# Kernel tuning notes

Hardware: AMD Instinct MI355X
Metric: run time of the kernel (lower is better)

## Reference

```python
import jax, jax.numpy as jnp
import numpy as np
from jax import lax

B, C, H, W = 8, 128, 256, 256
Q = 3            # polynomial order of SuperONN2d
K = 3            # kernel size
OC = C // 2      # SuperONN2d out channels
EPS = 1e-5       # LayerNorm eps (torch default)


def setup_inputs() -> dict:
    key = jax.random.key(0)
    k1, k2, k3 = jax.random.split(key, 3)
    x = jax.random.normal(k1, (B, C, H, W), dtype=jnp.float32)
    gamma = jnp.ones((C,), dtype=jnp.float32)
    beta = jnp.zeros((C,), dtype=jnp.float32)
    # SuperONN2d weight: (out_ch, q*in_ch, k, k), bias=False
    fan_in = Q * C * K * K
    Wc = jax.random.uniform(k2, (OC, Q * C, K, K), dtype=jnp.float32,
                            minval=-1.0, maxval=1.0) / np.sqrt(fan_in)
    return {"x": x, "gamma": gamma, "beta": beta, "Wc": Wc}


def _pixel_unshuffle2(y):
    # torch.nn.PixelUnshuffle(2): (B,C,H,W) -> (B,4C,H/2,W/2)
    b, c, h, w = y.shape
    y = y.reshape(b, c, h // 2, 2, w // 2, 2)
    y = y.transpose(0, 1, 3, 5, 2, 4)
    return y.reshape(b, c * 4, h // 2, w // 2)


def reference(x, gamma, beta, Wc):
    # LayerNormNLP2d: normalize over channel dim at each pixel
    mu = jnp.mean(x, axis=1, keepdims=True)
    var = jnp.mean(jnp.square(x - mu), axis=1, keepdims=True)
    xn = (x - mu) * lax.rsqrt(var + EPS)
    xn = xn * gamma[None, :, None, None] + beta[None, :, None, None]
    # SuperONN2d: concat powers x^1..x^Q on channels, then a single conv (no bias)
    xp = jnp.concatenate([xn ** (i + 1) for i in range(Q)], axis=1)  # (B, Q*C, H, W)
    y = lax.conv_general_dilated(
        xp, Wc, window_strides=(1, 1), padding=[(K // 2, K // 2)] * 2,
        dimension_numbers=("NCHW", "OIHW", "NCHW"))                  # (B, OC, H, W)
    return _pixel_unshuffle2(y)                                       # (B, 2C, H/2, W/2)
```

## Files before the change

kernel.cpp:

```cpp
#include <hip/hip_runtime.h>
#include <hip/hip_bf16.h>
#include <stdint.h>

#define BB   8
#define CCH  128
#define HH   256
#define WWD  256
#define OCC  64
#define HWW  (HH*WWD)
#define PLANE (BB*HWW*32)

typedef __attribute__((ext_vector_type(8)))  short  bf16x8;
typedef __attribute__((ext_vector_type(16))) float  f32x16;
typedef __attribute__((ext_vector_type(4)))  unsigned int u32x4;
typedef __attribute__((ext_vector_type(2)))  float  f32x2;

static __device__ __forceinline__ unsigned cvt_pk_bf16(float lo, float hi) {
    unsigned r;
    asm("v_cvt_pk_bf16_f32 %0, %1, %2" : "=v"(r) : "v"(lo), "v"(hi));
    return r;
}
static __device__ __forceinline__ float bf16lo_to_f(unsigned u) {
    union { unsigned u; float f; } c; c.u = u << 16; return c.f;
}
static __device__ __forceinline__ float bf16hi_to_f(unsigned u) {
    union { unsigned u; float f; } c; c.u = u & 0xffff0000u; return c.f;
}

__global__ void prep_w(const float* __restrict__ Wc, unsigned short* __restrict__ Wb3) {
    int t = blockIdx.x * 256 + threadIdx.x;
    int lane = t & 63;
    int f    = t >> 6;
    int nt   = f & 1;
    int kh   = (f >> 1) & 1;
    int cc   = (f >> 2) & 3;
    int tq   = f >> 4;
    int q    = tq % 3;
    int tap  = tq / 3;
    int oc   = nt * 32 + (lane & 31);
    int kb   = cc * 32 + kh * 16 + (lane >> 5) * 8;
    u32x4 o;
    #pragma unroll
    for (int k = 0; k < 4; ++k) {
        float v0 = Wc[(size_t)(oc * 384 + q * 128 + kb + 2 * k) * 9 + tap];
        float v1 = Wc[(size_t)(oc * 384 + q * 128 + kb + 2 * k + 1) * 9 + tap];
        o[k] = cvt_pk_bf16(v0, v1);
    }
    *(u32x4*)(Wb3 + (size_t)t * 8) = o;
}

__global__ __launch_bounds__(256) void ln_kernel(
        const float* __restrict__ x, const float* __restrict__ gamma,
        const float* __restrict__ beta, unsigned short* __restrict__ xn2) {
    int p  = blockIdx.x * 256 + threadIdx.x;
    int b  = p >> 16;
    int hw = p & 65535;
    const float* xb = x + (size_t)b * CCH * HWW + hw;
    unsigned buf[64];
    float sum = 0.f, sumsq = 0.f;
    #pragma unroll
    for (int cp = 0; cp < 64; ++cp) {
        float v0 = xb[(size_t)(2 * cp) * HWW];
        float v1 = xb[(size_t)(2 * cp + 1) * HWW];
        sum   += v0 + v1;
        sumsq += v0 * v0 + v1 * v1;
        buf[cp] = cvt_pk_bf16(v0, v1);
    }
    float mu  = sum * (1.f / 128.f);
    float var = sumsq * (1.f / 128.f) - mu * mu;
    float rs  = rsqrtf(var + 1e-5f);
    size_t pix = (size_t)p * 32;
    #pragma unroll
    for (int g = 0; g < 16; ++g) {
        u32x4 o;
        #pragma unroll
        for (int k = 0; k < 4; ++k) {
            int cp = g * 4 + k;
            float f0 = bf16lo_to_f(buf[cp]);
            float f1 = bf16hi_to_f(buf[cp]);
            int c0 = cp * 2, c1 = cp * 2 + 1;
            float y0 = fmaf((f0 - mu) * rs, gamma[c0], beta[c0]);
            float y1 = fmaf((f1 - mu) * rs, gamma[c1], beta[c1]);
            o[k] = cvt_pk_bf16(y0, y1);
        }
        *(u32x4*)(xn2 + (size_t)(g >> 2) * PLANE + pix + (g & 3) * 8) = o;
    }
}

__global__ __launch_bounds__(256, 2) void conv_kernel(
        const unsigned short* __restrict__ xn2,
        const unsigned short* __restrict__ Wb3,
        float* __restrict__ out) {
    __shared__ __align__(16) unsigned char P[10 * 12 * 34 * 16];

    int bid = blockIdx.x;
    int bx  = bid & 7;
    int by  = (bid >> 3) & 31;
    int b   = bid >> 8;
    int x0  = bx * 32;
    int y0  = by * 8;
    int tid  = threadIdx.x;
    int lane = tid & 63;
    int w    = tid >> 6;
    int l31  = lane & 31;
    int kb   = lane >> 5;

    f32x16 acc[2][2];
    #pragma unroll
    for (int mt = 0; mt < 2; ++mt)
        #pragma unroll
        for (int nt = 0; nt < 2; ++nt)
            #pragma unroll
            for (int r = 0; r < 16; ++r)
                acc[mt][nt][r] = 0.f;

    int offg[6];
    int woff[6];
    bool vldf[6], wrf[6];
    #pragma unroll
    for (int it = 0; it < 6; ++it) {
        int item = tid + it * 256;
        bool ok  = item < 1360;
        int ii   = ok ? item : 0;
        int row  = ii / 136;
        int rem  = ii - row * 136;
        int px   = rem >> 2;
        int g2   = rem & 3;
        int yy   = y0 - 1 + row;
        int xx   = x0 - 1 + px;
        bool inb = ok && (unsigned)yy < 256u && (unsigned)xx < 256u;
        offg[it] = (yy * 256 + xx) * 32 + g2 * 8;
        woff[it] = (row * 12 + g2) * 34 + px;
        vldf[it] = inb;
        wrf[it]  = ok;
    }

    const unsigned short* xpb = xn2 + (size_t)b * HWW * 32;
    const bf16x8* wlane = (const bf16x8*)Wb3 + lane;
    const unsigned char* pa = P + ((size_t)kb * 34 + l31) * 16;

    u32x4 rs[6];
    #pragma unroll
    for (int it = 0; it < 6; ++it) {
        u32x4 v = (u32x4){0u, 0u, 0u, 0u};
        if (vldf[it]) v = *(const u32x4*)(xpb + offg[it]);
        rs[it] = v;
    }

    #pragma unroll 1
    for (int cc = 0; cc < 4; ++cc) {
        if (cc > 0) __syncthreads();
        #pragma unroll
        for (int it = 0; it < 6; ++it) {
            if (!wrf[it]) continue;
            u32x4 u1 = rs[it];
            u32x4 u2, u3;
            #pragma unroll
            for (int k = 0; k < 4; ++k) {
                float f0 = bf16lo_to_f(u1[k]);
                float f1 = bf16hi_to_f(u1[k]);
                float s0 = f0 * f0, s1 = f1 * f1;
                u2[k] = cvt_pk_bf16(s0, s1);
                u3[k] = cvt_pk_bf16(s0 * f0, s1 * f1);
            }
            unsigned char* cell = P + (size_t)woff[it] * 16;
            *(u32x4*)(cell)            = u1;
            *(u32x4*)(cell + 4*34*16)  = u2;
            *(u32x4*)(cell + 8*34*16)  = u3;
        }
        __syncthreads();

        if (cc < 3) {
            const unsigned short* xpn = xpb + (size_t)(cc + 1) * PLANE;
            #pragma unroll
            for (int it = 0; it < 6; ++it) {
                u32x4 v = (u32x4){0u, 0u, 0u, 0u};
                if (vldf[it]) v = *(const u32x4*)(xpn + offg[it]);
                rs[it] = v;
            }
        }

        const bf16x8* wcc = wlane + (size_t)cc * 4 * 64;
        bf16x8 av[2][2][2], bv[2][2][2];
        #pragma unroll
        for (int mt = 0; mt < 2; ++mt)
            #pragma unroll
            for (int kh = 0; kh < 2; ++kh)
                av[0][mt][kh] = *(const bf16x8*)(pa
                    + (size_t)(((2 * w + mt) * 12 + kh * 2) * 34) * 16);
        #pragma unroll
        for (int nt = 0; nt < 2; ++nt)
            #pragma unroll
            for (int kh = 0; kh < 2; ++kh)
                bv[0][nt][kh] = wcc[(kh * 2 + nt) * 64];

        #pragma unroll
        for (int tq = 0; tq < 27; ++tq) {
            const int cur = tq & 1, nxt = cur ^ 1;
            if (tq < 26) {
                const int t2 = tq + 1;
                const int ky = t2 / 9, kx = (t2 / 3) % 3, q = t2 % 3;
                #pragma unroll
                for (int mt = 0; mt < 2; ++mt)
                    #pragma unroll
                    for (int kh = 0; kh < 2; ++kh)
                        av[nxt][mt][kh] = *(const bf16x8*)(pa
                            + (size_t)((((2 * w + mt + ky) * 12 + q * 4 + kh * 2) * 34)
                                       + kx) * 16);
                #pragma unroll
                for (int nt = 0; nt < 2; ++nt)
                    #pragma unroll
                    for (int kh = 0; kh < 2; ++kh)
                        bv[nxt][nt][kh] = wcc[((size_t)t2 * 16 + kh * 2 + nt) * 64];
            }
            __builtin_amdgcn_s_setprio(1);
            #pragma unroll
            for (int kh = 0; kh < 2; ++kh)
                #pragma unroll
                for (int nt = 0; nt < 2; ++nt)
                    #pragma unroll
                    for (int mt = 0; mt < 2; ++mt)
                        acc[mt][nt] = __builtin_amdgcn_mfma_f32_32x32x16_bf16(
                            av[cur][mt][kh], bv[cur][nt][kh], acc[mt][nt], 0, 0, 0);
            __builtin_amdgcn_s_setprio(0);
        }
    }

    #pragma unroll
    for (int mt = 0; mt < 2; ++mt) {
        int y  = y0 + 2 * w + mt;
        int s  = mt;
        int y2 = y >> 1;
        #pragma unroll
        for (int nt = 0; nt < 2; ++nt) {
            int oc = nt * 32 + l31;
            #pragma unroll
            for (int p = 0; p < 8; ++p) {
                const int r  = (p & 1) + (p >> 1) * 4;
                int px = (r & 3) + 8 * (r >> 2) + 4 * kb;
                int x  = x0 + px;
                int ch = oc * 4 + s * 2 + (x & 1);
                int x2 = x >> 1;
                size_t off = ((size_t)(b * 256 + ch) * 128 + y2) * 128 + x2;
                f32x2 v;
                v.x = acc[mt][nt][r];
                v.y = acc[mt][nt][r + 2];
                *(f32x2*)(out + off) = v;
            }
        }
    }
}

extern "C" void kernel_launch(void* const* d_in, const int* in_sizes, int n_in,
                              void* d_out, int out_size, void* d_ws, size_t ws_size,
                              hipStream_t stream) {
    const float* x     = (const float*)d_in[0];
    const float* gamma = (const float*)d_in[1];
    const float* beta  = (const float*)d_in[2];
    const float* Wc    = (const float*)d_in[3];
    float* out = (float*)d_out;

    const size_t xn_bytes = (size_t)4 * PLANE * 2;
    const size_t wb_bytes = (size_t)27648 * 16;
    if (ws_size < xn_bytes + wb_bytes) return;
    unsigned short* xn2 = (unsigned short*)d_ws;
    unsigned short* Wb3 = (unsigned short*)((char*)d_ws + xn_bytes);

    hipLaunchKernelGGL(prep_w, dim3(108), dim3(256), 0, stream, Wc, Wb3);
    hipLaunchKernelGGL(ln_kernel, dim3(2048), dim3(256), 0, stream, x, gamma, beta, xn2);
    hipLaunchKernelGGL(conv_kernel, dim3(2048), dim3(256), 0, stream, xn2, Wb3, out);
}
```

Before: 326.1 us.

## Use taller conv tiles with 16-channel sub-chunks for more weight reuse

The conv tile grows from 8 to 16 output rows per block, and each wave now handles 4 M-tiles instead of 2, so every weight B-fragment feeds 4 MFMAs. Channel chunks shrink from 32 to 16 so the LDS halo tile stays about the same size. The weight prepack layout is reordered to match, and the grid is halved. The aim is less halo reloading and less weight traffic per output. The cost is more accumulator registers, twice as many barriers and fill phases, and fewer blocks, which may hurt occupancy or latency hiding.

```diff
diff --git a/kernel.cpp b/kernel.cpp
--- a/kernel.cpp
+++ b/kernel.cpp
@@ -9,6 +9,8 @@
 #define OCC  64
 #define HWW  (HH*WWD)
 #define PLANE (BB*HWW*32)
+#define NLD  1224
+#define QSTR (2*34)
 
 typedef __attribute__((ext_vector_type(8)))  short  bf16x8;
 typedef __attribute__((ext_vector_type(16))) float  f32x16;
@@ -27,26 +29,25 @@
     union { unsigned u; float f; } c; c.u = u & 0xffff0000u; return c.f;
 }
 
-__global__ void prep_w(const float* __restrict__ Wc, unsigned short* __restrict__ Wb3) {
+__global__ void prep_w(const float* __restrict__ Wc, unsigned short* __restrict__ Wb4) {
     int t = blockIdx.x * 256 + threadIdx.x;
     int lane = t & 63;
     int f    = t >> 6;
     int nt   = f & 1;
-    int kh   = (f >> 1) & 1;
-    int cc   = (f >> 2) & 3;
+    int sc   = (f >> 1) & 7;
     int tq   = f >> 4;
     int q    = tq % 3;
     int tap  = tq / 3;
     int oc   = nt * 32 + (lane & 31);
-    int kb   = cc * 32 + kh * 16 + (lane >> 5) * 8;
+    int cb   = sc * 16 + (lane >> 5) * 8;
     u32x4 o;
     #pragma unroll
     for (int k = 0; k < 4; ++k) {
-        float v0 = Wc[(size_t)(oc * 384 + q * 128 + kb + 2 * k) * 9 + tap];
-        float v1 = Wc[(size_t)(oc * 384 + q * 128 + kb + 2 * k + 1) * 9 + tap];
+        float v0 = Wc[(size_t)(oc * 384 + q * 128 + cb + 2 * k) * 9 + tap];
+        float v1 = Wc[(size_t)(oc * 384 + q * 128 + cb + 2 * k + 1) * 9 + tap];
         o[k] = cvt_pk_bf16(v0, v1);
     }
-    *(u32x4*)(Wb3 + (size_t)t * 8) = o;
+    *(u32x4*)(Wb4 + (size_t)t * 8) = o;
 }
 
 __global__ __launch_bounds__(256) void ln_kernel(
@@ -89,71 +90,71 @@
 
 __global__ __launch_bounds__(256, 2) void conv_kernel(
         const unsigned short* __restrict__ xn2,
-        const unsigned short* __restrict__ Wb3,
+        const unsigned short* __restrict__ Wb4,
         float* __restrict__ out) {
-    __shared__ __align__(16) unsigned char P[10 * 12 * 34 * 16];
+    __shared__ __align__(16) unsigned char P[18 * 6 * 34 * 16];
 
     int bid = blockIdx.x;
     int bx  = bid & 7;
-    int by  = (bid >> 3) & 31;
-    int b   = bid >> 8;
+    int by  = (bid >> 3) & 15;
+    int b   = bid >> 7;
     int x0  = bx * 32;
-    int y0  = by * 8;
+    int y0  = by * 16;
     int tid  = threadIdx.x;
     int lane = tid & 63;
     int w    = tid >> 6;
     int l31  = lane & 31;
     int kb   = lane >> 5;
 
-    f32x16 acc[2][2];
-    #pragma unroll
-    for (int mt = 0; mt < 2; ++mt)
+    f32x16 acc[4][2];
+    #pragma unroll
+    for (int mt = 0; mt < 4; ++mt)
         #pragma unroll
         for (int nt = 0; nt < 2; ++nt)
             #pragma unroll
             for (int r = 0; r < 16; ++r)
                 acc[mt][nt][r] = 0.f;
 
-    int offg[6];
-    int woff[6];
-    bool vldf[6], wrf[6];
-    #pragma unroll
-    for (int it = 0; it < 6; ++it) {
+    int offg[5];
+    int woff[5];
+    bool vldf[5], wrf[5];
+    #pragma unroll
+    for (int it = 0; it < 5; ++it) {
         int item = tid + it * 256;
-        bool ok  = item < 1360;
+        bool ok  = item < NLD;
         int ii   = ok ? item : 0;
-        int row  = ii / 136;
-        int rem  = ii - row * 136;
-        int px   = rem >> 2;
-        int g2   = rem & 3;
+        int row  = ii / 68;
+        int rem  = ii - row * 68;
+        int g    = rem / 34;
+        int px   = rem - g * 34;
         int yy   = y0 - 1 + row;
         int xx   = x0 - 1 + px;
         bool inb = ok && (unsigned)yy < 256u && (unsigned)xx < 256u;
-        offg[it] = (yy * 256 + xx) * 32 + g2 * 8;
-        woff[it] = (row * 12 + g2) * 34 + px;
+        offg[it] = (yy * 256 + xx) * 32 + g * 8;
+        woff[it] = (row * 6 + g) * 34 + px;
         vldf[it] = inb;
         wrf[it]  = ok;
     }
 
     const unsigned short* xpb = xn2 + (size_t)b * HWW * 32;
-    const bf16x8* wlane = (const bf16x8*)Wb3 + lane;
+    const bf16x8* wlane = (const bf16x8*)Wb4 + lane;
     const unsigned char* pa = P + ((size_t)kb * 34 + l31) * 16;
 
-    u32x4 rs[6];
-    #pragma unroll
-    for (int it = 0; it < 6; ++it) {
+    u32x4 rsv[5];
+    #pragma unroll
+    for (int it = 0; it < 5; ++it) {
         u32x4 v = (u32x4){0u, 0u, 0u, 0u};
         if (vldf[it]) v = *(const u32x4*)(xpb + offg[it]);
-        rs[it] = v;
+        rsv[it] = v;
     }
 
     #pragma unroll 1
-    for (int cc = 0; cc < 4; ++cc) {
-        if (cc > 0) __syncthreads();
-        #pragma unroll
-        for (int it = 0; it < 6; ++it) {
+    for (int sc = 0; sc < 8; ++sc) {
+        if (sc > 0) __syncthreads();
+        #pragma unroll
+        for (int it = 0; it < 5; ++it) {
             if (!wrf[it]) continue;
-            u32x4 u1 = rs[it];
+            u32x4 u1 = rsv[it];
             u32x4 u2, u3;
             #pragma unroll
             for (int k = 0; k < 4; ++k) {
@@ -164,35 +165,32 @@
                 u3[k] = cvt_pk_bf16(s0 * f0, s1 * f1);
             }
             unsigned char* cell = P + (size_t)woff[it] * 16;
-            *(u32x4*)(cell)            = u1;
-            *(u32x4*)(cell + 4*34*16)  = u2;
-            *(u32x4*)(cell + 8*34*16)  = u3;
+            *(u32x4*)(cell)                  = u1;
+            *(u32x4*)(cell + QSTR * 16)      = u2;
+            *(u32x4*)(cell + 2 * QSTR * 16)  = u3;
         }
         __syncthreads();
 
-        if (cc < 3) {
-            const unsigned short* xpn = xpb + (size_t)(cc + 1) * PLANE;
-            #pragma unroll
-            for (int it = 0; it < 6; ++it) {
+        if (sc < 7) {
+            const int scn = sc + 1;
+            const unsigned short* xpn = xpb + (size_t)(scn >> 1) * PLANE
+                                            + (scn & 1) * 16;
+            #pragma unroll
+            for (int it = 0; it < 5; ++it) {
                 u32x4 v = (u32x4){0u, 0u, 0u, 0u};
                 if (vldf[it]) v = *(const u32x4*)(xpn + offg[it]);
-                rs[it] = v;
-            }
-        }
-
-        const bf16x8* wcc = wlane + (size_t)cc * 4 * 64;
-        bf16x8 av[2][2][2], bv[2][2][2];
-        #pragma unroll
-        for (int mt = 0; mt < 2; ++mt)
-            #pragma unroll
-            for (int kh = 0; kh < 2; ++kh)
-                av[0][mt][kh] = *(const bf16x8*)(pa
-                    + (size_t)(((2 * w + mt) * 12 + kh * 2) * 34) * 16);
+                rsv[it] = v;
+            }
+        }
+
+        const bf16x8* wsc = wlane + (size_t)sc * 2 * 64;
+        bf16x8 av[2][4], bv[2][2];
+        #pragma unroll
+        for (int mt = 0; mt < 4; ++mt)
+            av[0][mt] = *(const bf16x8*)(pa + (size_t)((4 * w + mt) * 6 * 34) * 16);
         #pragma unroll
         for (int nt = 0; nt < 2; ++nt)
-            #pragma unroll
-            for (int kh = 0; kh < 2; ++kh)
-                bv[0][nt][kh] = wcc[(kh * 2 + nt) * 64];
+            bv[0][nt] = wsc[nt * 64];
 
         #pragma unroll
         for (int tq = 0; tq < 27; ++tq) {
@@ -201,35 +199,28 @@
                 const int t2 = tq + 1;
                 const int ky = t2 / 9, kx = (t2 / 3) % 3, q = t2 % 3;
                 #pragma unroll
-                for (int mt = 0; mt < 2; ++mt)
-                    #pragma unroll
-                    for (int kh = 0; kh < 2; ++kh)
-                        av[nxt][mt][kh] = *(const bf16x8*)(pa
-                            + (size_t)((((2 * w + mt + ky) * 12 + q * 4 + kh * 2) * 34)
-                                       + kx) * 16);
+                for (int mt = 0; mt < 4; ++mt)
+                    av[nxt][mt] = *(const bf16x8*)(pa
+                        + (size_t)(((4 * w + mt + ky) * 6 + q * 2) * 34 + kx) * 16);
                 #pragma unroll
                 for (int nt = 0; nt < 2; ++nt)
-                    #pragma unroll
-                    for (int kh = 0; kh < 2; ++kh)
-                        bv[nxt][nt][kh] = wcc[((size_t)t2 * 16 + kh * 2 + nt) * 64];
+                    bv[nxt][nt] = wsc[((size_t)t2 * 16 + nt) * 64];
             }
             __builtin_amdgcn_s_setprio(1);
             #pragma unroll
-            for (int kh = 0; kh < 2; ++kh)
+            for (int nt = 0; nt < 2; ++nt)
                 #pragma unroll
-                for (int nt = 0; nt < 2; ++nt)
-                    #pragma unroll
-                    for (int mt = 0; mt < 2; ++mt)
-                        acc[mt][nt] = __builtin_amdgcn_mfma_f32_32x32x16_bf16(
-                            av[cur][mt][kh], bv[cur][nt][kh], acc[mt][nt], 0, 0, 0);
+                for (int mt = 0; mt < 4; ++mt)
+                    acc[mt][nt] = __builtin_amdgcn_mfma_f32_32x32x16_bf16(
+                        av[cur][mt], bv[cur][nt], acc[mt][nt], 0, 0, 0);
             __builtin_amdgcn_s_setprio(0);
         }
     }
 
     #pragma unroll
-    for (int mt = 0; mt < 2; ++mt) {
-        int y  = y0 + 2 * w + mt;
-        int s  = mt;
+    for (int mt = 0; mt < 4; ++mt) {
+        int y  = y0 + 4 * w + mt;
+        int s  = mt & 1;
         int y2 = y >> 1;
         #pragma unroll
         for (int nt = 0; nt < 2; ++nt) {
@@ -264,9 +255,9 @@
     const size_t wb_bytes = (size_t)27648 * 16;
     if (ws_size < xn_bytes + wb_bytes) return;
     unsigned short* xn2 = (unsigned short*)d_ws;
-    unsigned short* Wb3 = (unsigned short*)((char*)d_ws + xn_bytes);
-
-    hipLaunchKernelGGL(prep_w, dim3(108), dim3(256), 0, stream, Wc, Wb3);
+    unsigned short* Wb4 = (unsigned short*)((char*)d_ws + xn_bytes);
+
+    hipLaunchKernelGGL(prep_w, dim3(108), dim3(256), 0, stream, Wc, Wb4);
     hipLaunchKernelGGL(ln_kernel, dim3(2048), dim3(256), 0, stream, x, gamma, beta, xn2);
-    hipLaunchKernelGGL(conv_kernel, dim3(2048), dim3(256), 0, stream, xn2, Wb3, out);
-}
+    hipLaunchKernelGGL(conv_kernel, dim3(1024), dim3(256), 0, stream, xn2, Wb4, out);
+}
```

After: 326.7 us. Within noise of the previous version (+0.2%).
